# Optimization experiments

Hardware: AMD Instinct MI355X
Metric: run time of the kernel (lower is better)

The kernel has to match this reference:

```python
import jax, jax.numpy as jnp
import numpy as np

N_NODES = 100000
N_EDGES = 1600000
IN_DIM = 16
HID = 128
N_LAYERS = 3
LN_EPS = 1e-5


def setup_inputs() -> dict:
    key = jax.random.key(0)
    ks = jax.random.split(key, 8)
    x = jax.random.normal(ks[0], (N_NODES, IN_DIM), dtype=jnp.float32)
    edge_index = jax.random.randint(ks[1], (2, N_EDGES), 0, N_NODES, dtype=jnp.int64)
    # input projection params
    W_in = jax.random.normal(ks[2], (IN_DIM, HID), dtype=jnp.float32) * (1.0 / np.sqrt(IN_DIM))
    b_in = jnp.zeros((HID,), dtype=jnp.float32)
    # stacked GCNConv weights [L, H, H] and biases [L, H]
    W_conv = jax.random.normal(ks[3], (N_LAYERS, HID, HID), dtype=jnp.float32) * (1.0 / np.sqrt(HID))
    b_conv = jnp.zeros((N_LAYERS, HID), dtype=jnp.float32)
    # LayerNorm params [L, H]
    ln_gamma = jnp.ones((N_LAYERS, HID), dtype=jnp.float32)
    ln_beta = jnp.zeros((N_LAYERS, HID), dtype=jnp.float32)
    return {"x": x, "edge_index": edge_index, "W_in": W_in, "b_in": b_in,
            "W_conv": W_conv, "b_conv": b_conv, "ln_gamma": ln_gamma, "ln_beta": ln_beta}


def _layer_norm(h, gamma, beta):
    mu = jnp.mean(h, axis=-1, keepdims=True)
    var = jnp.mean(jnp.square(h - mu), axis=-1, keepdims=True)
    return (h - mu) * jax.lax.rsqrt(var + LN_EPS) * gamma + beta


def reference(x, edge_index, W_in, b_in, W_conv, b_conv, ln_gamma, ln_beta):
    N = x.shape[0]
    loops = jnp.arange(N, dtype=edge_index.dtype)
    src = jnp.concatenate([edge_index[0], loops])  # add self-loops (GCNConv default)
    dst = jnp.concatenate([edge_index[1], loops])
    # symmetric normalization D^-1/2 (A+I) D^-1/2
    deg = jax.ops.segment_sum(jnp.ones(src.shape[0], dtype=x.dtype), dst, num_segments=N)
    dis = jax.lax.rsqrt(jnp.maximum(deg, 1.0))  # deg >= 1 with self-loops
    coef = (dis[src] * dis[dst])[:, None]  # [E+N, 1]
    h = x @ W_in + b_in  # input projection -> [N, HID]
    for l in range(N_LAYERS):
        h_prev = h
        m = h @ W_conv[l]  # transform then propagate (same math as GCNConv)
        agg = jax.ops.segment_sum(m[src] * coef, dst, num_segments=N) + b_conv[l]
        h = jax.nn.relu(_layer_norm(agg, ln_gamma[l], ln_beta[l]))
        if l > 0:  # residual only for i > 0, dims always match
            h = h + h_prev
    return h
```

## Files before the change

kernel.cpp:

```cpp
#include <hip/hip_runtime.h>
#include <hip/hip_bf16.h>
#include <hip/hip_fp16.h>

#define HID 128
#define BCHUNK 4096

typedef __attribute__((ext_vector_type(8))) short short8;
typedef __attribute__((ext_vector_type(4))) float f32x4;

__device__ __forceinline__ float ldf(const void* p, size_t i, int bf16f) {
    if (bf16f) {
        unsigned short u = ((const unsigned short*)p)[i];
        union { unsigned int x; float f; } v; v.x = ((unsigned int)u) << 16;
        return v.f;
    }
    return ((const float*)p)[i];
}
__device__ __forceinline__ int ld_idx(const void* p, size_t i, int i64f) {
    return i64f ? (int)((const long long*)p)[i] : ((const int*)p)[i];
}
__device__ __forceinline__ unsigned short f2bfu(float f) {
    __hip_bfloat16 h = __float2bfloat16(f);
    return *reinterpret_cast<unsigned short*>(&h);
}
__device__ __forceinline__ float bflo(unsigned int u) {
    union { unsigned int x; float f; } v; v.x = u << 16;
    return v.f;
}
__device__ __forceinline__ float bfhi(unsigned int u) {
    union { unsigned int x; float f; } v; v.x = u & 0xffff0000u;
    return v.f;
}

__global__ void k_init(const void* __restrict__ gamma, const void* __restrict__ ei,
                       int* flags, int* bkcur, int nbk) {
    int t = threadIdx.x;
    for (int i = t; i < nbk; i += 256) bkcur[i] = 0;
    if (t == 0) {
        unsigned int g0 = ((const unsigned int*)gamma)[0];
        flags[0] = (g0 != 0x3F800000u) ? 1 : 0;
        const unsigned int* e32 = (const unsigned int*)ei;
        int i64 = 1;
        for (int k = 0; k < 128; k++)
            if (e32[2 * k + 1] != 0u) { i64 = 0; break; }
        flags[1] = i64;
    }
}

__global__ __launch_bounds__(256) void k_bucket(const void* __restrict__ ei,
                                                int E, int N, int nbk, int cap,
                                                int* bkcur, unsigned* __restrict__ bdata,
                                                const int* __restrict__ flags) {
    __shared__ int hist[512], base[512];
    int i64 = flags[1];
    int t = threadIdx.x;
    for (int i = t; i < nbk; i += 256) hist[i] = 0;
    __syncthreads();
    int e0 = blockIdx.x * BCHUNK;
    int ss[16], dd[16];
#pragma unroll
    for (int k = 0; k < 16; k++) {
        int e = e0 + k * 256 + t;
        dd[k] = -1;
        if (e < E) {
            int d = ld_idx(ei, (size_t)E + e, i64);
            int s = ld_idx(ei, e, i64);
            if ((unsigned)d < (unsigned)N && (unsigned)s < (unsigned)N) {
                dd[k] = d; ss[k] = s;
                atomicAdd(&hist[d >> 9], 1);
            }
        }
    }
    __syncthreads();
    for (int i = t; i < nbk; i += 256) {
        int c = hist[i];
        base[i] = c ? atomicAdd(&bkcur[i], c) : 0;
        hist[i] = 0;
    }
    __syncthreads();
#pragma unroll
    for (int k = 0; k < 16; k++) {
        if (dd[k] >= 0) {
            int b = dd[k] >> 9;
            int pos = base[b] + atomicAdd(&hist[b], 1);
            if (pos < cap)
                bdata[(size_t)b * cap + pos] =
                    (unsigned)ss[k] | ((unsigned)(dd[k] & 511) << 17);
        }
    }
}

__global__ __launch_bounds__(256) void k_bfused(const int* __restrict__ bkcur,
                                                const unsigned* __restrict__ bdata,
                                                int cap, int* __restrict__ row_ptr,
                                                float* __restrict__ dis,
                                                int* __restrict__ csr_src,
                                                int N, int nbk) {
    __shared__ int hist[512];
    __shared__ int sb[256];
    __shared__ int lsum, bkbase;
    int b = blockIdx.x, t = threadIdx.x;
    int bv = (t < nbk) ? min(bkcur[t], cap) : 0;
    sb[t] = bv;
    __syncthreads();
    int acc = bv;
    for (int off = 1; off < 256; off <<= 1) {
        int x = (t >= off) ? sb[t - off] : 0;
        __syncthreads();
        acc += x; sb[t] = acc;
        __syncthreads();
    }
    if (t == b) bkbase = acc - bv;
    if (b == nbk - 1 && t == nbk - 1) row_ptr[N] = acc;
    for (int i = t; i < 512; i += 256) hist[i] = 0;
    __syncthreads();
    int cb = min(bkcur[b], cap);
    for (int k = t; k < cb; k += 256)
        atomicAdd(&hist[bdata[(size_t)b * cap + k] >> 17], 1);
    __syncthreads();
    int v0 = hist[t], v1 = hist[256 + t];
    int s0 = v0, s1 = v1;
    for (int off = 1; off < 256; off <<= 1) {
        int x0 = (t >= off) ? hist[t - off] : 0;
        int x1 = (t >= off) ? hist[256 + t - off] : 0;
        __syncthreads();
        s0 += x0; s1 += x1;
        hist[t] = s0; hist[256 + t] = s1;
        __syncthreads();
    }
    if (t == 255) lsum = s0;
    __syncthreads();
    int nbase = b << 9;
    int e0 = bkbase + s0 - v0;
    int e1 = bkbase + lsum + s1 - v1;
    if (nbase + t < N) {
        row_ptr[nbase + t] = e0;
        dis[nbase + t] = rsqrtf((float)(v0 + 1));
    }
    if (nbase + 256 + t < N) {
        row_ptr[nbase + 256 + t] = e1;
        dis[nbase + 256 + t] = rsqrtf((float)(v1 + 1));
    }
    __syncthreads();
    hist[t] = e0; hist[256 + t] = e1;
    __syncthreads();
    for (int k = t; k < cb; k += 256) {
        unsigned u = bdata[(size_t)b * cap + k];
        int j = atomicAdd(&hist[u >> 17], 1);
        csr_src[j] = (int)(u & 0x1FFFFu);
    }
}

__global__ void k_proj(const void* __restrict__ x, const void* __restrict__ Win,
                       const void* __restrict__ bin,
                       unsigned short* __restrict__ hb, int N,
                       const void* __restrict__ Wc, unsigned short* __restrict__ Wt,
                       const int* __restrict__ flags) {
    int bf = flags[0];
    int t = threadIdx.x;
    if (blockIdx.x >= N) {
        int i = blockIdx.x - N;
        int l = i >> 7, n = i & 127;
        float w = ldf(Wc, (size_t)l * 16384 + (size_t)t * 128 + n, bf);
        Wt[(size_t)l * 16384 + (size_t)n * 128 + t] = f2bfu(w);
        return;
    }
    int node = blockIdx.x;
    __shared__ float xs[16];
    if (t < 16) xs[t] = ldf(x, (size_t)node * 16 + t, bf);
    __syncthreads();
    float acc = ldf(bin, t, bf);
#pragma unroll
    for (int k = 0; k < 16; k++)
        acc += xs[k] * ldf(Win, (size_t)k * HID + t, bf);
    hb[(size_t)node * HID + t] = f2bfu(acc);
}

__global__ __launch_bounds__(256) void k_gemm(const unsigned short* __restrict__ hb,
                                              const unsigned short* __restrict__ Wt,
                                              const float* __restrict__ dis,
                                              unsigned short* __restrict__ m, int N,
                                              int ntiles) {
    int t = threadIdx.x;
    int wave = t >> 6, lane = t & 63;
    int quad = lane >> 4, n15 = lane & 15;
    short8 bfr[4][8];
#pragma unroll
    for (int kc = 0; kc < 4; kc++)
#pragma unroll
        for (int nt = 0; nt < 8; nt++)
            bfr[kc][nt] = *(const short8*)(Wt + (size_t)(nt * 16 + n15) * HID +
                                           kc * 32 + quad * 8);
    int wid = blockIdx.x * 4 + wave;
    int nwaves = gridDim.x * 4;
    for (int tile = wid; tile < ntiles; tile += nwaves) {
        int row0 = tile * 16;
        int node = row0 + n15;
        int arow = min(node, N - 1);
        const short8* ap = (const short8*)(hb + (size_t)arow * HID + quad * 8);
        short8 a0 = ap[0], a1 = ap[4], a2 = ap[8], a3 = ap[12];
        float dn = dis[arow];
        f32x4 acc[8] = {};
#pragma unroll
        for (int nt = 0; nt < 8; nt++) {
            acc[nt] = __builtin_amdgcn_mfma_f32_16x16x32_bf16(bfr[0][nt], a0, acc[nt], 0, 0, 0);
            acc[nt] = __builtin_amdgcn_mfma_f32_16x16x32_bf16(bfr[1][nt], a1, acc[nt], 0, 0, 0);
            acc[nt] = __builtin_amdgcn_mfma_f32_16x16x32_bf16(bfr[2][nt], a2, acc[nt], 0, 0, 0);
            acc[nt] = __builtin_amdgcn_mfma_f32_16x16x32_bf16(bfr[3][nt], a3, acc[nt], 0, 0, 0);
        }
        if (node < N) {
            unsigned short* mp = m + (size_t)node * HID + quad * 4;
#pragma unroll
            for (int nt = 0; nt < 8; nt++) {
                unsigned lo = (unsigned)f2bfu(acc[nt][0] * dn) |
                              ((unsigned)f2bfu(acc[nt][1] * dn) << 16);
                unsigned hi = (unsigned)f2bfu(acc[nt][2] * dn) |
                              ((unsigned)f2bfu(acc[nt][3] * dn) << 16);
                *(uint2*)(mp + nt * 16) = make_uint2(lo, hi);
            }
        }
    }
}

__global__ __launch_bounds__(256) void k_layer(
        const int* __restrict__ row_ptr, const int* __restrict__ csr_src,
        const unsigned int* __restrict__ m2, const float* __restrict__ dis,
        const void* __restrict__ bc, size_t boff,
        const void* __restrict__ lg, const void* __restrict__ lb, size_t goff,
        unsigned int* __restrict__ hb, void* __restrict__ out, int N,
        int res, int last, const int* __restrict__ flags) {
    int t = threadIdx.x, wave = t >> 6, lane = t & 63;
    int node = blockIdx.x * 4 + wave;
    if (node >= N) return;
    int bf = flags[0];
    float dn = dis[node];
    unsigned int ms = m2[(unsigned)(node * 64 + lane)];
    float v0 = bflo(ms), v1 = bfhi(ms);
    int beg = row_ptr[node], end = row_ptr[node + 1];
    float p0 = 0.f, p1 = 0.f, q0 = 0.f, q1 = 0.f, r0 = 0.f, r1 = 0.f;
    int j = beg;
    for (; j + 3 < end; j += 4) {
        int s0 = csr_src[j], s1 = csr_src[j + 1];
        int s2 = csr_src[j + 2], s3 = csr_src[j + 3];
        unsigned int u0 = m2[(unsigned)(s0 * 64 + lane)];
        unsigned int u1 = m2[(unsigned)(s1 * 64 + lane)];
        unsigned int u2 = m2[(unsigned)(s2 * 64 + lane)];
        unsigned int u3 = m2[(unsigned)(s3 * 64 + lane)];
        v0 += bflo(u0); v1 += bfhi(u0);
        p0 += bflo(u1); p1 += bfhi(u1);
        q0 += bflo(u2); q1 += bfhi(u2);
        r0 += bflo(u3); r1 += bfhi(u3);
    }
    for (; j < end; j++) {
        int s0 = csr_src[j];
        unsigned int u0 = m2[(unsigned)(s0 * 64 + lane)];
        v0 += bflo(u0); v1 += bfhi(u0);
    }
    v0 += p0 + q0 + r0;
    v1 += p1 + q1 + r1;
    v0 = ldf(bc, boff + 2 * lane, bf) + v0 * dn;
    v1 = ldf(bc, boff + 2 * lane + 1, bf) + v1 * dn;
    float s1 = v0 + v1, s2 = v0 * v0 + v1 * v1;
#pragma unroll
    for (int o = 32; o; o >>= 1) {
        s1 += __shfl_down(s1, o);
        s2 += __shfl_down(s2, o);
    }
    float sum = __shfl(s1, 0), sq = __shfl(s2, 0);
    float mu = sum * (1.0f / HID);
    float var = sq * (1.0f / HID) - mu * mu;
    float r = rsqrtf(var + 1e-5f);
    float g0 = ldf(lg, goff + 2 * lane, bf), g1 = ldf(lg, goff + 2 * lane + 1, bf);
    float b0 = ldf(lb, goff + 2 * lane, bf), b1 = ldf(lb, goff + 2 * lane + 1, bf);
    float o0 = fmaxf((v0 - mu) * r * g0 + b0, 0.f);
    float o1 = fmaxf((v1 - mu) * r * g1 + b1, 0.f);
    size_t widx = (size_t)node * 64 + lane;
    if (res) {
        unsigned int hp = hb[widx];
        o0 += bflo(hp);
        o1 += bfhi(hp);
    }
    unsigned int packed = (unsigned int)f2bfu(o0) | ((unsigned int)f2bfu(o1) << 16);
    hb[widx] = packed;
    if (last) {
        if (bf) ((unsigned int*)out)[widx] = packed;
        else {
            size_t base = (size_t)node * HID + 2 * lane;
            *(float2*)&((float*)out)[base] = make_float2(o0, o1);
        }
    }
}

extern "C" void kernel_launch(void* const* d_in, const int* in_sizes, int n_in,
                              void* d_out, int out_size, void* d_ws, size_t ws_size,
                              hipStream_t stream) {
    const void* x   = d_in[0];
    const void* ei  = d_in[1];
    const void* Win = d_in[2];
    const void* bin = d_in[3];
    const void* Wc  = d_in[4];
    const void* bc  = d_in[5];
    const void* lg  = d_in[6];
    const void* lb  = d_in[7];

    int N = in_sizes[0] / 16;
    int E = in_sizes[1] / 2;
    int nbk = (N + 511) >> 9;
    int cap = ((E / nbk) * 2 + 255) & ~255;

    char* ws = (char*)d_ws;
    size_t off = 0;
    auto alloc = [&](size_t bytes) {
        void* p = ws + off;
        off += (bytes + 255) / 256 * 256;
        return p;
    };
    int*            flags    = (int*)alloc(256);
    float*          dis      = (float*)alloc((size_t)N * 4);
    int*            row_ptr  = (int*)alloc(((size_t)N + 1) * 4);
    int*            bkcur    = (int*)alloc((size_t)nbk * 4);
    unsigned*       bdata    = (unsigned*)alloc((size_t)nbk * cap * 4);
    int*            csr_src  = (int*)alloc((size_t)E * 4);
    unsigned short* hb       = (unsigned short*)alloc((size_t)N * HID * 2);
    unsigned short* m        = (unsigned short*)alloc((size_t)N * HID * 2);
    unsigned short* Wt       = (unsigned short*)alloc((size_t)3 * HID * HID * 2);
    (void)ws_size;

    k_init<<<1, 256, 0, stream>>>(lg, ei, flags, bkcur, nbk);
    k_bucket<<<(E + BCHUNK - 1) / BCHUNK, 256, 0, stream>>>(ei, E, N, nbk, cap,
                                                            bkcur, bdata, flags);
    k_bfused<<<nbk, 256, 0, stream>>>(bkcur, bdata, cap, row_ptr, dis, csr_src,
                                      N, nbk);
    k_proj<<<N + 3 * HID, HID, 0, stream>>>(x, Win, bin, hb, N, Wc, Wt, flags);

    int ntiles = (N + 15) / 16;
    int lblocks = (N + 3) / 4;
    for (int l = 0; l < 3; l++) {
        k_gemm<<<512, 256, 0, stream>>>(hb, Wt + (size_t)l * HID * HID, dis, m, N,
                                        ntiles);
        k_layer<<<lblocks, 256, 0, stream>>>(row_ptr, csr_src,
                                             (const unsigned int*)m, dis, bc,
                                             (size_t)l * HID, lg, lb, (size_t)l * HID,
                                             (unsigned int*)hb, d_out, N,
                                             l > 0, l == 2, flags);
    }
}
```

Baseline: 489.8 us.

## Make GCN aggregation kernel persistent with 8-wide unroll and prefetched neighbor indices

The per-node aggregation kernel becomes a grid-stride persistent kernel capped at 2048 blocks. Bias and LayerNorm parameters are hoisted out of the node loop, and node and row bounds are made wave-uniform with readfirstlane. The gather loop is unrolled to 8 neighbors, with the next 8 indices prefetched while the current rows load, and the tail is handled by clamped, masked loads. This aims to raise memory-level parallelism and cut per-node launch overhead, at the cost of more registers and some wasted tail loads. The csr_src buffer is padded so the over-reads stay in bounds.

```diff
diff --git a/kernel.cpp b/kernel.cpp
--- a/kernel.cpp
+++ b/kernel.cpp
@@ -230,63 +230,120 @@
         unsigned int* __restrict__ hb, void* __restrict__ out, int N,
         int res, int last, const int* __restrict__ flags) {
     int t = threadIdx.x, wave = t >> 6, lane = t & 63;
-    int node = blockIdx.x * 4 + wave;
-    if (node >= N) return;
+    int wid = blockIdx.x * 4 + wave;
+    int nwaves = gridDim.x * 4;
     int bf = flags[0];
-    float dn = dis[node];
-    unsigned int ms = m2[(unsigned)(node * 64 + lane)];
-    float v0 = bflo(ms), v1 = bfhi(ms);
-    int beg = row_ptr[node], end = row_ptr[node + 1];
-    float p0 = 0.f, p1 = 0.f, q0 = 0.f, q1 = 0.f, r0 = 0.f, r1 = 0.f;
-    int j = beg;
-    for (; j + 3 < end; j += 4) {
-        int s0 = csr_src[j], s1 = csr_src[j + 1];
-        int s2 = csr_src[j + 2], s3 = csr_src[j + 3];
-        unsigned int u0 = m2[(unsigned)(s0 * 64 + lane)];
-        unsigned int u1 = m2[(unsigned)(s1 * 64 + lane)];
-        unsigned int u2 = m2[(unsigned)(s2 * 64 + lane)];
-        unsigned int u3 = m2[(unsigned)(s3 * 64 + lane)];
-        v0 += bflo(u0); v1 += bfhi(u0);
-        p0 += bflo(u1); p1 += bfhi(u1);
-        q0 += bflo(u2); q1 += bfhi(u2);
-        r0 += bflo(u3); r1 += bfhi(u3);
-    }
-    for (; j < end; j++) {
-        int s0 = csr_src[j];
-        unsigned int u0 = m2[(unsigned)(s0 * 64 + lane)];
-        v0 += bflo(u0); v1 += bfhi(u0);
-    }
-    v0 += p0 + q0 + r0;
-    v1 += p1 + q1 + r1;
-    v0 = ldf(bc, boff + 2 * lane, bf) + v0 * dn;
-    v1 = ldf(bc, boff + 2 * lane + 1, bf) + v1 * dn;
-    float s1 = v0 + v1, s2 = v0 * v0 + v1 * v1;
-#pragma unroll
-    for (int o = 32; o; o >>= 1) {
-        s1 += __shfl_down(s1, o);
-        s2 += __shfl_down(s2, o);
-    }
-    float sum = __shfl(s1, 0), sq = __shfl(s2, 0);
-    float mu = sum * (1.0f / HID);
-    float var = sq * (1.0f / HID) - mu * mu;
-    float r = rsqrtf(var + 1e-5f);
+    float bb0 = ldf(bc, boff + 2 * lane, bf), bb1 = ldf(bc, boff + 2 * lane + 1, bf);
     float g0 = ldf(lg, goff + 2 * lane, bf), g1 = ldf(lg, goff + 2 * lane + 1, bf);
-    float b0 = ldf(lb, goff + 2 * lane, bf), b1 = ldf(lb, goff + 2 * lane + 1, bf);
-    float o0 = fmaxf((v0 - mu) * r * g0 + b0, 0.f);
-    float o1 = fmaxf((v1 - mu) * r * g1 + b1, 0.f);
-    size_t widx = (size_t)node * 64 + lane;
-    if (res) {
-        unsigned int hp = hb[widx];
-        o0 += bflo(hp);
-        o1 += bfhi(hp);
-    }
-    unsigned int packed = (unsigned int)f2bfu(o0) | ((unsigned int)f2bfu(o1) << 16);
-    hb[widx] = packed;
-    if (last) {
-        if (bf) ((unsigned int*)out)[widx] = packed;
-        else {
-            size_t base = (size_t)node * HID + 2 * lane;
-            *(float2*)&((float*)out)[base] = make_float2(o0, o1);
+    float be0 = ldf(lb, goff + 2 * lane, bf), be1 = ldf(lb, goff + 2 * lane + 1, bf);
+    unsigned lim = (unsigned)(N - 1);
+
+    for (int node = wid; node < N; node += nwaves) {
+        int nodeu = __builtin_amdgcn_readfirstlane(node);
+        float dn = dis[nodeu];
+        unsigned int ms = m2[(unsigned)(nodeu * 64) + lane];
+        float v0 = bflo(ms), v1 = bfhi(ms);
+        int begu = __builtin_amdgcn_readfirstlane(row_ptr[nodeu]);
+        int endu = __builtin_amdgcn_readfirstlane(row_ptr[nodeu + 1]);
+        float p0 = 0.f, p1 = 0.f, q0 = 0.f, q1 = 0.f, r0 = 0.f, r1 = 0.f;
+        int j = begu;
+        int c0 = 0, c1 = 0, c2 = 0, c3 = 0, c4 = 0, c5 = 0, c6 = 0, c7 = 0;
+        if (j + 7 < endu) {
+            c0 = csr_src[j];     c1 = csr_src[j + 1];
+            c2 = csr_src[j + 2]; c3 = csr_src[j + 3];
+            c4 = csr_src[j + 4]; c5 = csr_src[j + 5];
+            c6 = csr_src[j + 6]; c7 = csr_src[j + 7];
+        }
+        while (j + 7 < endu) {
+            unsigned int u0 = m2[(unsigned)(c0 * 64) + lane];
+            unsigned int u1 = m2[(unsigned)(c1 * 64) + lane];
+            unsigned int u2 = m2[(unsigned)(c2 * 64) + lane];
+            unsigned int u3 = m2[(unsigned)(c3 * 64) + lane];
+            unsigned int u4 = m2[(unsigned)(c4 * 64) + lane];
+            unsigned int u5 = m2[(unsigned)(c5 * 64) + lane];
+            unsigned int u6 = m2[(unsigned)(c6 * 64) + lane];
+            unsigned int u7 = m2[(unsigned)(c7 * 64) + lane];
+            int jn = j + 8;
+            int pj = min(jn, max(endu - 8, begu));
+            int n0 = csr_src[pj],     n1 = csr_src[pj + 1];
+            int n2 = csr_src[pj + 2], n3 = csr_src[pj + 3];
+            int n4 = csr_src[pj + 4], n5 = csr_src[pj + 5];
+            int n6 = csr_src[pj + 6], n7 = csr_src[pj + 7];
+            v0 += bflo(u0); v1 += bfhi(u0);
+            p0 += bflo(u1); p1 += bfhi(u1);
+            q0 += bflo(u2); q1 += bfhi(u2);
+            r0 += bflo(u3); r1 += bfhi(u3);
+            v0 += bflo(u4); v1 += bfhi(u4);
+            p0 += bflo(u5); p1 += bfhi(u5);
+            q0 += bflo(u6); q1 += bfhi(u6);
+            r0 += bflo(u7); r1 += bfhi(u7);
+            c0 = n0; c1 = n1; c2 = n2; c3 = n3;
+            c4 = n4; c5 = n5; c6 = n6; c7 = n7;
+            j = jn;
+        }
+        if (j < endu) {
+            int s0 = (int)min((unsigned)csr_src[j],     lim);
+            int s1 = (int)min((unsigned)csr_src[j + 1], lim);
+            int s2 = (int)min((unsigned)csr_src[j + 2], lim);
+            int s3 = (int)min((unsigned)csr_src[j + 3], lim);
+            int s4 = (int)min((unsigned)csr_src[j + 4], lim);
+            int s5 = (int)min((unsigned)csr_src[j + 5], lim);
+            int s6 = (int)min((unsigned)csr_src[j + 6], lim);
+            int s7 = (int)min((unsigned)csr_src[j + 7], lim);
+            unsigned int u0 = m2[(unsigned)(s0 * 64) + lane];
+            unsigned int u1 = m2[(unsigned)(s1 * 64) + lane];
+            unsigned int u2 = m2[(unsigned)(s2 * 64) + lane];
+            unsigned int u3 = m2[(unsigned)(s3 * 64) + lane];
+            unsigned int u4 = m2[(unsigned)(s4 * 64) + lane];
+            unsigned int u5 = m2[(unsigned)(s5 * 64) + lane];
+            unsigned int u6 = m2[(unsigned)(s6 * 64) + lane];
+            unsigned int u7 = m2[(unsigned)(s7 * 64) + lane];
+            u1 = (j + 1 < endu) ? u1 : 0u;
+            u2 = (j + 2 < endu) ? u2 : 0u;
+            u3 = (j + 3 < endu) ? u3 : 0u;
+            u4 = (j + 4 < endu) ? u4 : 0u;
+            u5 = (j + 5 < endu) ? u5 : 0u;
+            u6 = (j + 6 < endu) ? u6 : 0u;
+            u7 = (j + 7 < endu) ? u7 : 0u;
+            v0 += bflo(u0); v1 += bfhi(u0);
+            p0 += bflo(u1); p1 += bfhi(u1);
+            q0 += bflo(u2); q1 += bfhi(u2);
+            r0 += bflo(u3); r1 += bfhi(u3);
+            v0 += bflo(u4); v1 += bfhi(u4);
+            p0 += bflo(u5); p1 += bfhi(u5);
+            q0 += bflo(u6); q1 += bfhi(u6);
+            r0 += bflo(u7); r1 += bfhi(u7);
+        }
+        v0 += p0 + q0 + r0;
+        v1 += p1 + q1 + r1;
+        v0 = bb0 + v0 * dn;
+        v1 = bb1 + v1 * dn;
+        float s1 = v0 + v1, s2 = v0 * v0 + v1 * v1;
+#pragma unroll
+        for (int o = 32; o; o >>= 1) {
+            s1 += __shfl_down(s1, o);
+            s2 += __shfl_down(s2, o);
+        }
+        float sum = __shfl(s1, 0), sq = __shfl(s2, 0);
+        float mu = sum * (1.0f / HID);
+        float var = sq * (1.0f / HID) - mu * mu;
+        float r = rsqrtf(var + 1e-5f);
+        float o0 = fmaxf((v0 - mu) * r * g0 + be0, 0.f);
+        float o1 = fmaxf((v1 - mu) * r * g1 + be1, 0.f);
+        size_t widx = (size_t)nodeu * 64 + lane;
+        if (res) {
+            unsigned int hp = hb[widx];
+            o0 += bflo(hp);
+            o1 += bfhi(hp);
+        }
+        unsigned int packed = (unsigned int)f2bfu(o0) | ((unsigned int)f2bfu(o1) << 16);
+        hb[widx] = packed;
+        if (last) {
+            if (bf) ((unsigned int*)out)[widx] = packed;
+            else {
+                size_t base = (size_t)nodeu * HID + 2 * lane;
+                *(float2*)&((float*)out)[base] = make_float2(o0, o1);
+            }
         }
     }
 }
@@ -320,7 +377,7 @@
     int*            row_ptr  = (int*)alloc(((size_t)N + 1) * 4);
     int*            bkcur    = (int*)alloc((size_t)nbk * 4);
     unsigned*       bdata    = (unsigned*)alloc((size_t)nbk * cap * 4);
-    int*            csr_src  = (int*)alloc((size_t)E * 4);
+    int*            csr_src  = (int*)alloc((size_t)E * 4 + 64);
     unsigned short* hb       = (unsigned short*)alloc((size_t)N * HID * 2);
     unsigned short* m        = (unsigned short*)alloc((size_t)N * HID * 2);
     unsigned short* Wt       = (unsigned short*)alloc((size_t)3 * HID * HID * 2);
@@ -334,7 +391,7 @@
     k_proj<<<N + 3 * HID, HID, 0, stream>>>(x, Win, bin, hb, N, Wc, Wt, flags);
 
     int ntiles = (N + 15) / 16;
-    int lblocks = (N + 3) / 4;
+    int lblocks = min((N + 3) / 4, 2048);
     for (int l = 0; l < 3; l++) {
         k_gemm<<<512, 256, 0, stream>>>(hb, Wt + (size_t)l * HID * HID, dis, m, N,
                                         ntiles);
```

New measurement: 437.6 us. 1.12x faster.
